# Performance work log

Hardware: AMD Instinct MI355X
Metric: run time of the kernel (lower is better)

## Reference

```python
import jax, jax.numpy as jnp
import numpy as np

HIDDEN = 128
BSZ, C, Q = 8, 512, 64


def setup_inputs() -> dict:
    key = jax.random.key(0)
    k1, k2, k3, k4 = jax.random.split(key, 4)
    h = jax.random.normal(k1, (BSZ, C, HIDDEN), dtype=jnp.float32)
    u = jax.random.normal(k2, (BSZ, Q, HIDDEN), dtype=jnp.float32)
    # torch Linear stores weight as (out, in); xavier-uniform-like init
    lim1 = float(np.sqrt(6.0 / (3 * HIDDEN + HIDDEN)))
    w1 = jax.random.uniform(k3, (HIDDEN, 3 * HIDDEN), jnp.float32, -lim1, lim1)
    b1 = jnp.zeros((HIDDEN,), jnp.float32)
    lim2 = float(np.sqrt(6.0 / (HIDDEN + 1)))
    w2 = jax.random.uniform(k4, (1, HIDDEN), jnp.float32, -lim2, lim2)
    b2 = jnp.zeros((1,), jnp.float32)
    return {"h": h, "u": u, "w1": w1, "b1": b1, "w2": w2, "b2": b2}


def reference(h, u, w1, b1, w2, b2):
    # Decompose l1 weight into blocks acting on [h2, u2, h2*u2] so the
    # (bsz, C, Q, 3*hidden) concat tensor is never materialized.
    hid = h.shape[-1]
    w_h, w_u, w_hu = w1[:, :hid], w1[:, hid:2 * hid], w1[:, 2 * hid:]
    h_proj = jnp.einsum('bcd,kd->bck', h, w_h)          # (b, C, hidden)
    u_proj = jnp.einsum('bqd,kd->bqk', u, w_u)          # (b, Q, hidden)
    hu_proj = jnp.einsum('bcd,bqd,kd->bcqk', h, u, w_hu)  # (b, C, Q, hidden)
    l1 = jax.nn.relu(h_proj[:, :, None, :] + u_proj[:, None, :, :] + hu_proj + b1)
    l2 = jax.nn.relu(jnp.einsum('bcqk,ok->bcqo', l1, w2) + b2)
    out = jnp.squeeze(l2, axis=-1)  # (b, C, Q)
    if out.ndim == 2:  # bsz == 1 case in original
        out = out[None]
    return out
```

## Files before the change

### kernel.cpp

```cpp
#include <hip/hip_runtime.h>
#include <hip/hip_bf16.h>

typedef __bf16 bf16;
typedef __bf16 bf16x4 __attribute__((ext_vector_type(4)));
typedef __bf16 bf16x8 __attribute__((ext_vector_type(8)));
typedef float  f32x4  __attribute__((ext_vector_type(4)));

#define HID   128
#define BSZ   8
#define CDIM  512
#define QDIM  64
#define LDH   136

__global__ __launch_bounds__(256) __attribute__((amdgpu_waves_per_eu(2, 2)))
void sim_kernel(const float* __restrict__ hptr,
                const float* __restrict__ uptr,
                const float* __restrict__ w1,
                const float* __restrict__ b1,
                const float* __restrict__ w2,
                const float* __restrict__ b2,
                float* __restrict__ out)
{
    __shared__ __align__(16) bf16  weff[HID * LDH];
    __shared__ __align__(16) float ush[HID];
    __shared__ __align__(16) float bias_sh[HID];
    __shared__ __align__(16) float w2sh[HID];

    const int t  = threadIdx.x;
    const int bi = blockIdx.x & 7;
    const int qi = blockIdx.x >> 3;

    const float* uvec = uptr + (bi * QDIM + qi) * HID;

    if (t < HID) {
        ush[t]  = uvec[t];
        w2sh[t] = w2[t];
    }
    __syncthreads();

    {
        const int k     = t >> 1;
        const int dbase = (t & 1) * 64;
        const float* wrow = w1 + k * 384;
        #pragma unroll
        for (int j = 0; j < 16; ++j) {
            const int d = dbase + j * 4;
            float4 wh  = *(const float4*)(wrow + d);
            float4 whu = *(const float4*)(wrow + 256 + d);
            bf16x4 o;
            o[0] = (bf16)(wh.x + ush[d + 0] * whu.x);
            o[1] = (bf16)(wh.y + ush[d + 1] * whu.y);
            o[2] = (bf16)(wh.z + ush[d + 2] * whu.z);
            o[3] = (bf16)(wh.w + ush[d + 3] * whu.w);
            *(bf16x4*)&weff[k * LDH + d] = o;
        }
    }
    if (t < HID) {
        const float* wrow = w1 + t * 384 + 128;
        float acc = 0.f;
        #pragma unroll 8
        for (int d = 0; d < 128; d += 4) {
            float4 wu = *(const float4*)(wrow + d);
            acc += wu.x * ush[d] + wu.y * ush[d + 1] + wu.z * ush[d + 2] + wu.w * ush[d + 3];
        }
        bias_sh[t] = b1[t] + acc;
    }
    __syncthreads();

    const int lane = t & 63;
    const int wv   = t >> 6;
    const int col  = lane & 15;
    const int quad = lane >> 4;

    bf16x8 afrag[4][8];
    #pragma unroll
    for (int ks = 0; ks < 4; ++ks)
        #pragma unroll
        for (int mt = 0; mt < 8; ++mt)
            afrag[ks][mt] = *(const bf16x8*)&weff[(mt * 16 + col) * LDH + ks * 32 + quad * 8];

    f32x4 bias4[8], w24[8];
    #pragma unroll
    for (int mt = 0; mt < 8; ++mt) {
        bias4[mt] = *(const f32x4*)&bias_sh[mt * 16 + quad * 4];
        w24[mt]   = *(const f32x4*)&w2sh[mt * 16 + quad * 4];
    }
    const float b2v = b2[0];

    const float* hb    = hptr + bi * (CDIM * HID);
    float*       obase = out + (bi * CDIM) * QDIM + qi;

    for (int chunk = 0; chunk < 8; ++chunk) {
        const int c0 = wv * 128 + chunk * 16;
        const float* brow = hb + (c0 + col) * HID + quad * 8;

        f32x4 acc[8];
        #pragma unroll
        for (int mt = 0; mt < 8; ++mt) acc[mt] = bias4[mt];

        #pragma unroll
        for (int ks = 0; ks < 4; ++ks) {
            float4 v0 = *(const float4*)(brow + ks * 32);
            float4 v1 = *(const float4*)(brow + ks * 32 + 4);
            bf16x8 b;
            b[0] = (bf16)v0.x; b[1] = (bf16)v0.y; b[2] = (bf16)v0.z; b[3] = (bf16)v0.w;
            b[4] = (bf16)v1.x; b[5] = (bf16)v1.y; b[6] = (bf16)v1.z; b[7] = (bf16)v1.w;
            #pragma unroll
            for (int mt = 0; mt < 8; ++mt)
                acc[mt] = __builtin_amdgcn_mfma_f32_16x16x32_bf16(afrag[ks][mt], b, acc[mt], 0, 0, 0);
        }

        float s = 0.f;
        #pragma unroll
        for (int mt = 0; mt < 8; ++mt) {
            s += fmaxf(acc[mt][0], 0.f) * w24[mt][0];
            s += fmaxf(acc[mt][1], 0.f) * w24[mt][1];
            s += fmaxf(acc[mt][2], 0.f) * w24[mt][2];
            s += fmaxf(acc[mt][3], 0.f) * w24[mt][3];
        }
        s += __shfl_xor(s, 16, 64);
        s += __shfl_xor(s, 32, 64);
        if (lane < 16)
            obase[(c0 + col) * QDIM] = fmaxf(s + b2v, 0.f);
    }
}

extern "C" void kernel_launch(void* const* d_in, const int* in_sizes, int n_in,
                              void* d_out, int out_size, void* d_ws, size_t ws_size,
                              hipStream_t stream) {
    const float* h  = (const float*)d_in[0];
    const float* u  = (const float*)d_in[1];
    const float* w1 = (const float*)d_in[2];
    const float* b1 = (const float*)d_in[3];
    const float* w2 = (const float*)d_in[4];
    const float* b2 = (const float*)d_in[5];
    float* out = (float*)d_out;

    sim_kernel<<<dim3(BSZ * QDIM), dim3(256), 0, stream>>>(h, u, w1, b1, w2, b2, out);
}
```

Measured before the change: 91.74 us.

## Add prep kernel converting h to bf16 and precomputing per-query bias

Adds a prep kernel that converts h to bf16 once, interleaves the w_h and w_hu rows as bf16 pairs, and computes the u-projection bias for every (batch, query) with a shared-memory tiled dot product. The main kernel then streams half as many bytes of h per block, skips the per-block f32-to-bf16 conversion and the serial 128-thread bias loop, and reads its weights from the packed bf16 buffer. The cost is an extra kernel launch plus a workspace round-trip, and w_h and w_hu are now rounded to bf16 before the u-dependent combine.

```diff
diff --git a/kernel.cpp b/kernel.cpp
--- a/kernel.cpp
+++ b/kernel.cpp
@@ -12,58 +12,118 @@
 #define QDIM  64
 #define LDH   136
 
+#define HBF_OFF   0u
+#define WHHU_OFF  1048576u
+#define BIAS_OFF  1114112u
+
+__global__ __launch_bounds__(256)
+void prep_kernel(const float* __restrict__ hptr,
+                 const float* __restrict__ uptr,
+                 const float* __restrict__ w1,
+                 const float* __restrict__ b1,
+                 char* __restrict__ ws)
+{
+    const int t   = threadIdx.x;
+    const int blk = blockIdx.x;
+
+    if (blk < 128) {
+        bf16* hbf = (bf16*)(ws + HBF_OFF);
+        const int base4 = blk * 1024;
+        #pragma unroll
+        for (int i = 0; i < 4; ++i) {
+            const int f4 = base4 + i * 256 + t;
+            float4 v = *(const float4*)(hptr + f4 * 4);
+            bf16x4 o;
+            o[0] = (bf16)v.x; o[1] = (bf16)v.y; o[2] = (bf16)v.z; o[3] = (bf16)v.w;
+            *(bf16x4*)&hbf[f4 * 4] = o;
+        }
+    } else if (blk < 136) {
+        bf16* whhu = (bf16*)(ws + WHHU_OFF);
+        const int kg = blk - 128;
+        #pragma unroll
+        for (int i = 0; i < 8; ++i) {
+            const int idx = i * 256 + t;
+            const int kl = idx >> 7, d = idx & 127;
+            const int k  = kg * 16 + kl;
+            const float wh  = w1[k * 384 + d];
+            const float whu = w1[k * 384 + 256 + d];
+            bf16* p = &whhu[k * 256 + d * 2];
+            p[0] = (bf16)wh;
+            p[1] = (bf16)whu;
+        }
+    } else {
+        __shared__ float u_sh[QDIM * 132];
+        __shared__ float wu_sh[16 * 132];
+        const int id = blk - 136;
+        const int b  = id >> 3;
+        const int kg = id & 7;
+        const float* ub = uptr + b * QDIM * HID;
+        #pragma unroll
+        for (int i = 0; i < 8; ++i) {
+            const int f4 = i * 256 + t;
+            const int q = f4 >> 5, c4 = f4 & 31;
+            *(float4*)&u_sh[q * 132 + c4 * 4] = *(const float4*)(ub + f4 * 4);
+        }
+        #pragma unroll
+        for (int i = 0; i < 2; ++i) {
+            const int f4 = i * 256 + t;
+            const int r = f4 >> 5, c4 = f4 & 31;
+            *(float4*)&wu_sh[r * 132 + c4 * 4] =
+                *(const float4*)(w1 + (kg * 16 + r) * 384 + 128 + c4 * 4);
+        }
+        __syncthreads();
+        float* bias = (float*)(ws + BIAS_OFF);
+        #pragma unroll
+        for (int i = 0; i < 4; ++i) {
+            const int p = i * 256 + t;
+            const int q = p >> 4, kk = p & 15;
+            const float* uu = &u_sh[q * 132];
+            const float* wu = &wu_sh[kk * 132];
+            float acc = 0.f;
+            #pragma unroll 8
+            for (int d = 0; d < 128; d += 4) {
+                f32x4 a = *(const f32x4*)&uu[d];
+                f32x4 w = *(const f32x4*)&wu[d];
+                acc += a[0]*w[0] + a[1]*w[1] + a[2]*w[2] + a[3]*w[3];
+            }
+            bias[(b * QDIM + q) * HID + kg * 16 + kk] = b1[kg * 16 + kk] + acc;
+        }
+    }
+}
+
 __global__ __launch_bounds__(256) __attribute__((amdgpu_waves_per_eu(2, 2)))
-void sim_kernel(const float* __restrict__ hptr,
+void sim_kernel(const char* __restrict__ ws,
                 const float* __restrict__ uptr,
-                const float* __restrict__ w1,
-                const float* __restrict__ b1,
                 const float* __restrict__ w2,
                 const float* __restrict__ b2,
                 float* __restrict__ out)
 {
     __shared__ __align__(16) bf16  weff[HID * LDH];
     __shared__ __align__(16) float ush[HID];
-    __shared__ __align__(16) float bias_sh[HID];
-    __shared__ __align__(16) float w2sh[HID];
 
     const int t  = threadIdx.x;
     const int bi = blockIdx.x & 7;
     const int qi = blockIdx.x >> 3;
 
     const float* uvec = uptr + (bi * QDIM + qi) * HID;
-
-    if (t < HID) {
-        ush[t]  = uvec[t];
-        w2sh[t] = w2[t];
-    }
+    if (t < HID) ush[t] = uvec[t];
     __syncthreads();
 
     {
+        const bf16* whhu = (const bf16*)(ws + WHHU_OFF);
         const int k     = t >> 1;
         const int dbase = (t & 1) * 64;
-        const float* wrow = w1 + k * 384;
         #pragma unroll
         for (int j = 0; j < 16; ++j) {
             const int d = dbase + j * 4;
-            float4 wh  = *(const float4*)(wrow + d);
-            float4 whu = *(const float4*)(wrow + 256 + d);
+            bf16x8 pw = *(const bf16x8*)(whhu + k * 256 + d * 2);
             bf16x4 o;
-            o[0] = (bf16)(wh.x + ush[d + 0] * whu.x);
-            o[1] = (bf16)(wh.y + ush[d + 1] * whu.y);
-            o[2] = (bf16)(wh.z + ush[d + 2] * whu.z);
-            o[3] = (bf16)(wh.w + ush[d + 3] * whu.w);
+            o[0] = (bf16)((float)pw[0] + ush[d + 0] * (float)pw[1]);
+            o[1] = (bf16)((float)pw[2] + ush[d + 1] * (float)pw[3]);
+            o[2] = (bf16)((float)pw[4] + ush[d + 2] * (float)pw[5]);
+            o[3] = (bf16)((float)pw[6] + ush[d + 3] * (float)pw[7]);
             *(bf16x4*)&weff[k * LDH + d] = o;
         }
-    }
-    if (t < HID) {
-        const float* wrow = w1 + t * 384 + 128;
-        float acc = 0.f;
-        #pragma unroll 8
-        for (int d = 0; d < 128; d += 4) {
-            float4 wu = *(const float4*)(wrow + d);
-            acc += wu.x * ush[d] + wu.y * ush[d + 1] + wu.z * ush[d + 2] + wu.w * ush[d + 3];
-        }
-        bias_sh[t] = b1[t] + acc;
     }
     __syncthreads();
 
@@ -79,20 +139,21 @@
         for (int mt = 0; mt < 8; ++mt)
             afrag[ks][mt] = *(const bf16x8*)&weff[(mt * 16 + col) * LDH + ks * 32 + quad * 8];
 
+    const float* bias_row = (const float*)(ws + BIAS_OFF) + (bi * QDIM + qi) * HID;
     f32x4 bias4[8], w24[8];
     #pragma unroll
     for (int mt = 0; mt < 8; ++mt) {
-        bias4[mt] = *(const f32x4*)&bias_sh[mt * 16 + quad * 4];
-        w24[mt]   = *(const f32x4*)&w2sh[mt * 16 + quad * 4];
+        bias4[mt] = *(const f32x4*)&bias_row[mt * 16 + quad * 4];
+        w24[mt]   = *(const f32x4*)&w2[mt * 16 + quad * 4];
     }
     const float b2v = b2[0];
 
-    const float* hb    = hptr + bi * (CDIM * HID);
-    float*       obase = out + (bi * CDIM) * QDIM + qi;
+    const bf16* hb    = (const bf16*)(ws + HBF_OFF) + bi * (CDIM * HID);
+    float*      obase = out + (bi * CDIM) * QDIM + qi;
 
     for (int chunk = 0; chunk < 8; ++chunk) {
         const int c0 = wv * 128 + chunk * 16;
-        const float* brow = hb + (c0 + col) * HID + quad * 8;
+        const bf16* brow = hb + (c0 + col) * HID + quad * 8;
 
         f32x4 acc[8];
         #pragma unroll
@@ -100,11 +161,7 @@
 
         #pragma unroll
         for (int ks = 0; ks < 4; ++ks) {
-            float4 v0 = *(const float4*)(brow + ks * 32);
-            float4 v1 = *(const float4*)(brow + ks * 32 + 4);
-            bf16x8 b;
-            b[0] = (bf16)v0.x; b[1] = (bf16)v0.y; b[2] = (bf16)v0.z; b[3] = (bf16)v0.w;
-            b[4] = (bf16)v1.x; b[5] = (bf16)v1.y; b[6] = (bf16)v1.z; b[7] = (bf16)v1.w;
+            bf16x8 b = *(const bf16x8*)(brow + ks * 32);
             #pragma unroll
             for (int mt = 0; mt < 8; ++mt)
                 acc[mt] = __builtin_amdgcn_mfma_f32_16x16x32_bf16(afrag[ks][mt], b, acc[mt], 0, 0, 0);
@@ -135,6 +192,8 @@
     const float* w2 = (const float*)d_in[4];
     const float* b2 = (const float*)d_in[5];
     float* out = (float*)d_out;
+    char*  ws  = (char*)d_ws;
 
-    sim_kernel<<<dim3(BSZ * QDIM), dim3(256), 0, stream>>>(h, u, w1, b1, w2, b2, out);
+    prep_kernel<<<dim3(200), dim3(256), 0, stream>>>(h, u, w1, b1, ws);
+    sim_kernel<<<dim3(BSZ * QDIM), dim3(256), 0, stream>>>(ws, u, w2, b2, out);
 }
```

New measurement: 83.47 us. -9.0%, faster.
